# Performance work log

Hardware: AMD Instinct MI355X
Metric: run time of the kernel (lower is better)

Reference implementation:

```python
import jax, jax.numpy as jnp
import numpy as np

H = 128  # DECODER_LAYERS[0]
LN_EPS = 1e-3  # keras LayerNormalization default epsilon


def setup_inputs() -> dict:
    key = jax.random.key(0)
    ks = jax.random.split(key, 12)
    N_POS, N_COL, D = 1024, 512, 128
    n_seq = 8
    s = 1.0 / np.sqrt(D)
    h = 1.0 / np.sqrt(H)
    return {
        "seq_feat": jax.random.normal(ks[0], (N_POS, D), jnp.float32),
        "col_feat": jax.random.normal(ks[1], (N_COL, D), jnp.float32),
        "sequence_lengths": jnp.full((n_seq,), N_POS // n_seq, dtype=jnp.int32),
        "Ws": jax.random.normal(ks[2], (D, H), jnp.float32) * s,
        "bs": jnp.zeros((H,), jnp.float32),
        "Wc": jax.random.normal(ks[3], (D, H), jnp.float32) * s,
        "bc": jnp.zeros((H,), jnp.float32),
        "Wm": jax.random.normal(ks[4], (H, H), jnp.float32) * h,
        "bm": jnp.zeros((H,), jnp.float32),
        "gamma": jnp.ones((H,), jnp.float32),
        "beta": jnp.zeros((H,), jnp.float32),
        "Wo": jax.random.normal(ks[5], (H, 1), jnp.float32) * h,
        "bo": jnp.zeros((1,), jnp.float32),
    }


def reference(seq_feat, col_feat, sequence_lengths, Ws, bs, Wc, bc, Wm, bm, gamma, beta, Wo, bo):
    N_POS = seq_feat.shape[0]
    N_COL = col_feat.shape[0]
    n_seq = sequence_lengths.shape[0]

    seq_dec = jax.nn.relu(seq_feat @ Ws + bs)   # [N_pos, H]
    col_dec = jax.nn.relu(col_feat @ Wc + bc)   # [N_col, H]

    # broadcast outer-sum: [N_pos, N_col, H]
    logits = seq_dec[:, None, :] + col_dec[None, :, :]

    # MLP([128]): single Dense (no activation) + LayerNorm
    hmid = logits @ Wm + bm
    mu = jnp.mean(hmid, axis=-1, keepdims=True)
    var = jnp.mean(jnp.square(hmid - mu), axis=-1, keepdims=True)
    hln = (hmid - mu) / jnp.sqrt(var + LN_EPS) * gamma + beta

    raw = (hln @ Wo + bo)[..., 0]               # [N_pos, N_col]
    exp_logits = jnp.exp(raw)

    # column-axis normalization (softmax over last axis)
    M_c = exp_logits / jnp.sum(exp_logits, axis=-1, keepdims=True)

    # segment-ragged normalization over positions, per sequence
    segment_ids = jnp.repeat(jnp.arange(n_seq, dtype=jnp.int32), sequence_lengths,
                             total_repeat_length=N_POS)
    seg = jax.ops.segment_sum(exp_logits, segment_ids, num_segments=n_seq)  # [n_seq, N_col]
    M_s = exp_logits / seg[segment_ids]

    return M_c + M_s - M_c * M_s
```

## Files before the change

### kernel.cpp

```cpp
#include <hip/hip_runtime.h>

#define HDIM 128
#define NPOS 1024
#define NCOL 512
#define LN_EPS 1e-3f


__device__ __forceinline__ int seg_of(int i, const int* __restrict__ lens, int n_seq) {
    int cum = 0;
    for (int s = 0; s < n_seq; ++s) {
        cum += lens[s];
        if (i < cum) return s;
    }
    return n_seq - 1;
}

extern "C" __global__ void __launch_bounds__(512)
k1_precompute(const float* __restrict__ seq_feat, const float* __restrict__ col_feat,
              const float* __restrict__ Ws, const float* __restrict__ bsv,
              const float* __restrict__ Wc, const float* __restrict__ bcv,
              const float* __restrict__ Wm, const float* __restrict__ bmv,
              const float* __restrict__ gam, const float* __restrict__ Wo,
              const int* __restrict__ lens, int n_seq,
              float* __restrict__ AcT, float* __restrict__ BcT,
              float* __restrict__ p_arr, float* __restrict__ v_arr,
              float* __restrict__ q_arr, float* __restrict__ w_arr,
              float* __restrict__ sums, int* __restrict__ segid)
{
    __shared__ float xs[4][HDIM];
    __shared__ float ds_[4][HDIM];
    __shared__ float partm[8], partp[8], partv[8], mus[4];

    const int t    = threadIdx.x;
    const int b    = blockIdx.x;
    const int h    = t & 127;
    const int r    = t >> 7;
    const int wv   = t >> 6;
    const int lane = t & 63;

    {
        const int nsums = NPOS + n_seq * NCOL;
        int idx = b * 512 + t;
        if (idx < nsums) sums[idx] = 0.f;
        int idx2 = idx - nsums;
        if (idx2 >= 0 && idx2 < NPOS) segid[idx2] = seg_of(idx2, lens, n_seq);
    }

    const bool  is_seq = (b < NPOS / 4);
    const int   i0 = (is_seq ? b : (b - NPOS / 4)) * 4;
    const float* X  = is_seq ? seq_feat : col_feat;
    const float* W1 = is_seq ? Ws : Wc;
    const float* b1 = is_seq ? bsv : bcv;

    if (t < 128) {
        int rr = t >> 5, k4 = (t & 31) * 4;
        *(float4*)&xs[rr][k4] = *(const float4*)&X[(i0 + rr) * HDIM + k4];
    }
    __syncthreads();

    float d;
    {
        float a0 = 0.f, a1 = 0.f, a2 = 0.f, a3 = 0.f;
        #pragma unroll 8
        for (int k = 0; k < HDIM; k += 4) {
            float4 x = *(const float4*)&xs[r][k];
            float w0 = W1[(k + 0) * HDIM + h];
            float w1 = W1[(k + 1) * HDIM + h];
            float w2 = W1[(k + 2) * HDIM + h];
            float w3 = W1[(k + 3) * HDIM + h];
            a0 += x.x * w0; a1 += x.y * w1; a2 += x.z * w2; a3 += x.w * w3;
        }
        d = fmaxf(b1[h] + ((a0 + a1) + (a2 + a3)), 0.f);
    }
    ds_[r][h] = d;
    __syncthreads();

    float aa;
    {
        float a0 = 0.f, a1 = 0.f, a2 = 0.f, a3 = 0.f;
        #pragma unroll 8
        for (int k = 0; k < HDIM; k += 4) {
            float4 x = *(const float4*)&ds_[r][k];
            float w0 = Wm[(k + 0) * HDIM + h];
            float w1 = Wm[(k + 1) * HDIM + h];
            float w2 = Wm[(k + 2) * HDIM + h];
            float w3 = Wm[(k + 3) * HDIM + h];
            a0 += x.x * w0; a1 += x.y * w1; a2 += x.z * w2; a3 += x.w * w3;
        }
        aa = (is_seq ? 0.f : bmv[h]) + ((a0 + a1) + (a2 + a3));
    }

    {
        float s = aa;
        #pragma unroll
        for (int off = 32; off; off >>= 1) s += __shfl_xor(s, off, 64);
        if (lane == 0) partm[wv] = s;
    }
    __syncthreads();
    if (t < 4) mus[t] = (partm[2 * t] + partm[2 * t + 1]) * (1.f / HDIM);
    __syncthreads();

    const float a  = aa - mus[r];
    const float gw = gam[h] * Wo[h];

    {
        float sp = a * gw, sv = a * a;
        #pragma unroll
        for (int off = 32; off; off >>= 1) {
            sp += __shfl_xor(sp, off, 64);
            sv += __shfl_xor(sv, off, 64);
        }
        if (lane == 0) { partp[wv] = sp; partv[wv] = sv; }
    }
    xs[r][h] = a;
    __syncthreads();
    if (t < 4) {
        (is_seq ? p_arr : q_arr)[i0 + t] = partp[2 * t] + partp[2 * t + 1];
        (is_seq ? v_arr : w_arr)[i0 + t] = (partv[2 * t] + partv[2 * t + 1]) * (1.f / HDIM);
    }
    if (t < 128) {
        float4 st = make_float4(xs[0][t], xs[1][t], xs[2][t], xs[3][t]);
        if (is_seq) *(float4*)&AcT[t * NPOS + i0] = st;
        else        *(float4*)&BcT[t * NCOL + i0] = st;
    }
}

#define AS_STR 36
#define BS_STR 68

union K2Smem {
    struct { float As[128 * AS_STR]; float Bs[128 * BS_STR]; } s;
    struct { float comb[8 * 256]; float redr[512]; float redc[1024]; } r;
};

extern "C" __global__ void __launch_bounds__(512)
k2_gemm(const float* __restrict__ AcT, const float* __restrict__ BcT,
        const float* __restrict__ p_arr, const float* __restrict__ v_arr,
        const float* __restrict__ q_arr, const float* __restrict__ w_arr,
        const int* __restrict__ segid, int n_seq,
        float* __restrict__ E, float* __restrict__ rowsum, float* __restrict__ segsum)
{
    __shared__ K2Smem sm;

    const int t  = threadIdx.x;
    const int tt = t & 255;
    const int tc = tt & 15;
    const int tr = tt >> 4;
    const int kbase = (t >> 8) * 64;
    const int i0 = blockIdx.x * 32;
    const int j0 = blockIdx.y * 64;

    #pragma unroll
    for (int u = 0; u < 2; ++u) {
        int fid = t + 512 * u;
        int k = fid >> 3, m4 = fid & 7;
        *(float4*)&sm.s.As[k * AS_STR + 4 * m4] = *(const float4*)&AcT[k * NPOS + i0 + 4 * m4];
    }
    #pragma unroll
    for (int u = 0; u < 4; ++u) {
        int fid = t + 512 * u;
        int k = fid >> 4, n4 = fid & 15;
        *(float4*)&sm.s.Bs[k * BS_STR + 4 * n4] = *(const float4*)&BcT[k * NCOL + j0 + 4 * n4];
    }
    __syncthreads();

    float acc[8] = {0.f, 0.f, 0.f, 0.f, 0.f, 0.f, 0.f, 0.f};
    #pragma unroll 4
    for (int k = kbase; k < kbase + 64; ++k) {
        float2 a2 = *(const float2*)&sm.s.As[k * AS_STR + 2 * tr];
        float4 b4 = *(const float4*)&sm.s.Bs[k * BS_STR + 4 * tc];
        acc[0] += a2.x * b4.x; acc[1] += a2.x * b4.y; acc[2] += a2.x * b4.z; acc[3] += a2.x * b4.w;
        acc[4] += a2.y * b4.x; acc[5] += a2.y * b4.y; acc[6] += a2.y * b4.z; acc[7] += a2.y * b4.w;
    }

    const int seg_lo = segid[i0];
    const int seg_hi = segid[i0 + 31];
    __syncthreads();

    if (t >= 256) {
        #pragma unroll
        for (int j = 0; j < 8; ++j) sm.r.comb[j * 256 + tt] = acc[j];
    }
    __syncthreads();

    float e[2][4];
    if (t < 256) {
        #pragma unroll
        for (int j = 0; j < 8; ++j) acc[j] += sm.r.comb[j * 256 + tt];

        const int jj = j0 + 4 * tc;
        float4 q4 = *(const float4*)&q_arr[jj];
        float4 w4 = *(const float4*)&w_arr[jj];
        float rs[2];
        #pragma unroll
        for (int mm = 0; mm < 2; ++mm) {
            const int i = i0 + 2 * tr + mm;
            const float pi = p_arr[i];
            const float vi = v_arr[i];
            e[mm][0] = __expf((pi + q4.x) * rsqrtf(vi + w4.x + acc[4*mm+0] * (2.f/HDIM) + LN_EPS));
            e[mm][1] = __expf((pi + q4.y) * rsqrtf(vi + w4.y + acc[4*mm+1] * (2.f/HDIM) + LN_EPS));
            e[mm][2] = __expf((pi + q4.z) * rsqrtf(vi + w4.z + acc[4*mm+2] * (2.f/HDIM) + LN_EPS));
            e[mm][3] = __expf((pi + q4.w) * rsqrtf(vi + w4.w + acc[4*mm+3] * (2.f/HDIM) + LN_EPS));
            rs[mm] = e[mm][0] + e[mm][1] + e[mm][2] + e[mm][3];
            *(float4*)&E[i * NCOL + jj] = make_float4(e[mm][0], e[mm][1], e[mm][2], e[mm][3]);
        }
        sm.r.redr[(2 * tr + 0) * 16 + tc] = rs[0];
        sm.r.redr[(2 * tr + 1) * 16 + tc] = rs[1];
        #pragma unroll
        for (int u = 0; u < 4; ++u)
            sm.r.redc[(4 * tc + u) * 16 + tr] = e[0][u] + e[1][u];
    }
    __syncthreads();

    if (t < 32) {
        float s = 0.f;
        #pragma unroll
        for (int m = 0; m < 16; ++m) s += sm.r.redr[t * 16 + m];
        atomicAdd(&rowsum[i0 + t], s);
    } else if (t >= 32 && t < 96 && seg_lo == seg_hi) {
        int c = t - 32;
        float s = 0.f;
        #pragma unroll
        for (int m = 0; m < 16; ++m) s += sm.r.redc[c * 16 + m];
        atomicAdd(&segsum[seg_lo * NCOL + j0 + c], s);
    }
    if (seg_lo != seg_hi && t < 256) {
        #pragma unroll
        for (int mm = 0; mm < 2; ++mm) {
            const int i = i0 + 2 * tr + mm;
            const int sg = segid[i];
            #pragma unroll
            for (int u = 0; u < 4; ++u)
                atomicAdd(&segsum[sg * NCOL + j0 + 4 * tc + u], e[mm][u]);
        }
    }
}

extern "C" __global__ void __launch_bounds__(256)
k3_final(const float* __restrict__ E, const float* __restrict__ rowsum,
         const float* __restrict__ segsum, const int* __restrict__ segid,
         float* __restrict__ out)
{
    const int gid = blockIdx.x * 256 + threadIdx.x;
    const int i = gid >> 7;
    const int j = (gid & 127) * 4;

    float4 e4 = *(const float4*)&E[i * NCOL + j];
    const float invr = 1.f / rowsum[i];
    const int sg = segid[i];
    float4 s4 = *(const float4*)&segsum[sg * NCOL + j];

    float4 o;
    { float mc = e4.x * invr, ms = e4.x / s4.x; o.x = mc + ms - mc * ms; }
    { float mc = e4.y * invr, ms = e4.y / s4.y; o.y = mc + ms - mc * ms; }
    { float mc = e4.z * invr, ms = e4.z / s4.z; o.z = mc + ms - mc * ms; }
    { float mc = e4.w * invr, ms = e4.w / s4.w; o.w = mc + ms - mc * ms; }
    *(float4*)&out[i * NCOL + j] = o;
}

extern "C" void kernel_launch(void* const* d_in, const int* in_sizes, int n_in,
                              void* d_out, int out_size, void* d_ws, size_t ws_size,
                              hipStream_t stream) {
    const float* seq_feat = (const float*)d_in[0];
    const float* col_feat = (const float*)d_in[1];
    const int*   lens     = (const int*)d_in[2];
    const float* Ws   = (const float*)d_in[3];
    const float* bs   = (const float*)d_in[4];
    const float* Wc   = (const float*)d_in[5];
    const float* bc   = (const float*)d_in[6];
    const float* Wm   = (const float*)d_in[7];
    const float* bm   = (const float*)d_in[8];
    const float* gam  = (const float*)d_in[9];
    const float* Wo   = (const float*)d_in[11];
    float* out = (float*)d_out;
    const int n_seq = in_sizes[2];

    float* ws     = (float*)d_ws;
    float* AcT    = ws;
    float* BcT    = AcT + HDIM * NPOS;
    float* p      = BcT + HDIM * NCOL;
    float* v      = p + NPOS;
    float* q      = v + NPOS;
    float* w      = q + NCOL;
    float* sums   = w + NCOL;
    float* rowsum = sums;
    float* segsum = sums + NPOS;
    float* E      = segsum + n_seq * NCOL;
    int*   segid  = (int*)(E + NPOS * NCOL);

    hipLaunchKernelGGL(k1_precompute, dim3(NPOS / 4 + NCOL / 4), dim3(512), 0, stream,
                       seq_feat, col_feat, Ws, bs, Wc, bc, Wm, bm, gam, Wo,
                       lens, n_seq, AcT, BcT, p, v, q, w, sums, segid);
    hipLaunchKernelGGL(k2_gemm, dim3(NPOS / 32, NCOL / 64), dim3(512), 0, stream,
                       AcT, BcT, p, v, q, w, segid, n_seq, E, rowsum, segsum);
    hipLaunchKernelGGL(k3_final, dim3((NPOS * NCOL / 4) / 256), dim3(256), 0, stream,
                       E, rowsum, segsum, segid, out);
}
```

Measured before the change: 98.59 us.

## Fuse three kernels into one persistent kernel with atomic grid barriers

Merges the precompute, GEMM/exp and final normalization kernels into a single 256-block kernel that separates phases with a spin-wait grid barrier on a global atomic counter, reset by a memset before launch. Phase 1 loops two passes over the row units so 256 blocks cover all 384. The aim is to remove the launch gaps between kernels. In exchange it adds a memset launch and barrier spin costs, and it depends on all 256 blocks being resident at once, with no cooperative-launch guarantee.

```diff
diff --git a/kernel.cpp b/kernel.cpp
--- a/kernel.cpp
+++ b/kernel.cpp
@@ -4,258 +4,269 @@
 #define NPOS 1024
 #define NCOL 512
 #define LN_EPS 1e-3f
-
-
-__device__ __forceinline__ int seg_of(int i, const int* __restrict__ lens, int n_seq) {
-    int cum = 0;
-    for (int s = 0; s < n_seq; ++s) {
-        cum += lens[s];
-        if (i < cum) return s;
-    }
-    return n_seq - 1;
-}
-
-extern "C" __global__ void __launch_bounds__(512)
-k1_precompute(const float* __restrict__ seq_feat, const float* __restrict__ col_feat,
-              const float* __restrict__ Ws, const float* __restrict__ bsv,
-              const float* __restrict__ Wc, const float* __restrict__ bcv,
-              const float* __restrict__ Wm, const float* __restrict__ bmv,
-              const float* __restrict__ gam, const float* __restrict__ Wo,
-              const int* __restrict__ lens, int n_seq,
-              float* __restrict__ AcT, float* __restrict__ BcT,
-              float* __restrict__ p_arr, float* __restrict__ v_arr,
-              float* __restrict__ q_arr, float* __restrict__ w_arr,
-              float* __restrict__ sums, int* __restrict__ segid)
-{
-    __shared__ float xs[4][HDIM];
-    __shared__ float ds_[4][HDIM];
-    __shared__ float partm[8], partp[8], partv[8], mus[4];
-
-    const int t    = threadIdx.x;
-    const int b    = blockIdx.x;
-    const int h    = t & 127;
-    const int r    = t >> 7;
-    const int wv   = t >> 6;
-    const int lane = t & 63;
-
-    {
-        const int nsums = NPOS + n_seq * NCOL;
-        int idx = b * 512 + t;
-        if (idx < nsums) sums[idx] = 0.f;
-        int idx2 = idx - nsums;
-        if (idx2 >= 0 && idx2 < NPOS) segid[idx2] = seg_of(idx2, lens, n_seq);
-    }
-
-    const bool  is_seq = (b < NPOS / 4);
-    const int   i0 = (is_seq ? b : (b - NPOS / 4)) * 4;
-    const float* X  = is_seq ? seq_feat : col_feat;
-    const float* W1 = is_seq ? Ws : Wc;
-    const float* b1 = is_seq ? bsv : bcv;
-
-    if (t < 128) {
-        int rr = t >> 5, k4 = (t & 31) * 4;
-        *(float4*)&xs[rr][k4] = *(const float4*)&X[(i0 + rr) * HDIM + k4];
-    }
-    __syncthreads();
-
-    float d;
-    {
-        float a0 = 0.f, a1 = 0.f, a2 = 0.f, a3 = 0.f;
-        #pragma unroll 8
-        for (int k = 0; k < HDIM; k += 4) {
-            float4 x = *(const float4*)&xs[r][k];
-            float w0 = W1[(k + 0) * HDIM + h];
-            float w1 = W1[(k + 1) * HDIM + h];
-            float w2 = W1[(k + 2) * HDIM + h];
-            float w3 = W1[(k + 3) * HDIM + h];
-            a0 += x.x * w0; a1 += x.y * w1; a2 += x.z * w2; a3 += x.w * w3;
-        }
-        d = fmaxf(b1[h] + ((a0 + a1) + (a2 + a3)), 0.f);
-    }
-    ds_[r][h] = d;
-    __syncthreads();
-
-    float aa;
-    {
-        float a0 = 0.f, a1 = 0.f, a2 = 0.f, a3 = 0.f;
-        #pragma unroll 8
-        for (int k = 0; k < HDIM; k += 4) {
-            float4 x = *(const float4*)&ds_[r][k];
-            float w0 = Wm[(k + 0) * HDIM + h];
-            float w1 = Wm[(k + 1) * HDIM + h];
-            float w2 = Wm[(k + 2) * HDIM + h];
-            float w3 = Wm[(k + 3) * HDIM + h];
-            a0 += x.x * w0; a1 += x.y * w1; a2 += x.z * w2; a3 += x.w * w3;
-        }
-        aa = (is_seq ? 0.f : bmv[h]) + ((a0 + a1) + (a2 + a3));
-    }
-
-    {
-        float s = aa;
-        #pragma unroll
-        for (int off = 32; off; off >>= 1) s += __shfl_xor(s, off, 64);
-        if (lane == 0) partm[wv] = s;
-    }
-    __syncthreads();
-    if (t < 4) mus[t] = (partm[2 * t] + partm[2 * t + 1]) * (1.f / HDIM);
-    __syncthreads();
-
-    const float a  = aa - mus[r];
-    const float gw = gam[h] * Wo[h];
-
-    {
-        float sp = a * gw, sv = a * a;
-        #pragma unroll
-        for (int off = 32; off; off >>= 1) {
-            sp += __shfl_xor(sp, off, 64);
-            sv += __shfl_xor(sv, off, 64);
-        }
-        if (lane == 0) { partp[wv] = sp; partv[wv] = sv; }
-    }
-    xs[r][h] = a;
-    __syncthreads();
-    if (t < 4) {
-        (is_seq ? p_arr : q_arr)[i0 + t] = partp[2 * t] + partp[2 * t + 1];
-        (is_seq ? v_arr : w_arr)[i0 + t] = (partv[2 * t] + partv[2 * t + 1]) * (1.f / HDIM);
-    }
-    if (t < 128) {
-        float4 st = make_float4(xs[0][t], xs[1][t], xs[2][t], xs[3][t]);
-        if (is_seq) *(float4*)&AcT[t * NPOS + i0] = st;
-        else        *(float4*)&BcT[t * NCOL + i0] = st;
-    }
-}
+#define NBLK 256
+
 
 #define AS_STR 36
 #define BS_STR 68
 
-union K2Smem {
+union FusedSmem {
+    struct {
+        float xs[4][HDIM];
+        float ds[4][HDIM];
+        float partm[8], partp[8], partv[8], mus[4];
+    } p1;
     struct { float As[128 * AS_STR]; float Bs[128 * BS_STR]; } s;
     struct { float comb[8 * 256]; float redr[512]; float redc[1024]; } r;
 };
 
-extern "C" __global__ void __launch_bounds__(512)
-k2_gemm(const float* __restrict__ AcT, const float* __restrict__ BcT,
-        const float* __restrict__ p_arr, const float* __restrict__ v_arr,
-        const float* __restrict__ q_arr, const float* __restrict__ w_arr,
-        const int* __restrict__ segid, int n_seq,
-        float* __restrict__ E, float* __restrict__ rowsum, float* __restrict__ segsum)
-{
-    __shared__ K2Smem sm;
-
-    const int t  = threadIdx.x;
-    const int tt = t & 255;
-    const int tc = tt & 15;
-    const int tr = tt >> 4;
-    const int kbase = (t >> 8) * 64;
-    const int i0 = blockIdx.x * 32;
-    const int j0 = blockIdx.y * 64;
-
-    #pragma unroll
-    for (int u = 0; u < 2; ++u) {
-        int fid = t + 512 * u;
-        int k = fid >> 3, m4 = fid & 7;
-        *(float4*)&sm.s.As[k * AS_STR + 4 * m4] = *(const float4*)&AcT[k * NPOS + i0 + 4 * m4];
-    }
-    #pragma unroll
-    for (int u = 0; u < 4; ++u) {
-        int fid = t + 512 * u;
-        int k = fid >> 4, n4 = fid & 15;
-        *(float4*)&sm.s.Bs[k * BS_STR + 4 * n4] = *(const float4*)&BcT[k * NCOL + j0 + 4 * n4];
+__device__ __forceinline__ int seg_of(int i, const int* __restrict__ lens, int n_seq) {
+    int cum = 0;
+    for (int s = 0; s < n_seq; ++s) { cum += lens[s]; if (i < cum) return s; }
+    return n_seq - 1;
+}
+
+__device__ __forceinline__ void grid_sync(unsigned int* bar, unsigned int need) {
+    __syncthreads();
+    if (threadIdx.x == 0) {
+        __hip_atomic_fetch_add(bar, 1u, __ATOMIC_RELEASE, __HIP_MEMORY_SCOPE_AGENT);
+        while (__hip_atomic_load(bar, __ATOMIC_ACQUIRE, __HIP_MEMORY_SCOPE_AGENT) < need) {}
     }
     __syncthreads();
-
-    float acc[8] = {0.f, 0.f, 0.f, 0.f, 0.f, 0.f, 0.f, 0.f};
-    #pragma unroll 4
-    for (int k = kbase; k < kbase + 64; ++k) {
-        float2 a2 = *(const float2*)&sm.s.As[k * AS_STR + 2 * tr];
-        float4 b4 = *(const float4*)&sm.s.Bs[k * BS_STR + 4 * tc];
-        acc[0] += a2.x * b4.x; acc[1] += a2.x * b4.y; acc[2] += a2.x * b4.z; acc[3] += a2.x * b4.w;
-        acc[4] += a2.y * b4.x; acc[5] += a2.y * b4.y; acc[6] += a2.y * b4.z; acc[7] += a2.y * b4.w;
+}
+
+extern "C" __global__ void __launch_bounds__(512, 2)
+fused_all(const float* __restrict__ seq_feat, const float* __restrict__ col_feat,
+          const float* __restrict__ Ws, const float* __restrict__ bsv,
+          const float* __restrict__ Wc, const float* __restrict__ bcv,
+          const float* __restrict__ Wm, const float* __restrict__ bmv,
+          const float* __restrict__ gam, const float* __restrict__ Wo,
+          const int* __restrict__ lens, int n_seq,
+          float* __restrict__ AcT, float* __restrict__ BcT,
+          float* __restrict__ p_arr, float* __restrict__ v_arr,
+          float* __restrict__ q_arr, float* __restrict__ w_arr,
+          float* __restrict__ sums, int* __restrict__ segid,
+          float* __restrict__ E, float* __restrict__ out,
+          unsigned int* __restrict__ bar)
+{
+    __shared__ FusedSmem sm;
+    const int t = threadIdx.x;
+    const int b = blockIdx.x;
+
+    {
+        const int h    = t & 127;
+        const int r    = t >> 7;
+        const int wv   = t >> 6;
+        const int lane = t & 63;
+
+        {
+            const int nsums = NPOS + n_seq * NCOL;
+            int idx = b * 512 + t;
+            if (idx < nsums) sums[idx] = 0.f;
+            int idx2 = idx - nsums;
+            if (idx2 >= 0 && idx2 < NPOS) segid[idx2] = seg_of(idx2, lens, n_seq);
+        }
+
+        for (int pass = 0; pass < 2; ++pass) {
+            const int unit = b + NBLK * pass;
+            if (unit < (NPOS + NCOL) / 4) {
+                const bool  is_seq = (unit < NPOS / 4);
+                const int   i0 = (is_seq ? unit : unit - NPOS / 4) * 4;
+                const float* X  = is_seq ? seq_feat : col_feat;
+                const float* W1 = is_seq ? Ws : Wc;
+                const float* b1 = is_seq ? bsv : bcv;
+
+                if (t < 128) {
+                    int rr = t >> 5, k4 = (t & 31) * 4;
+                    *(float4*)&sm.p1.xs[rr][k4] = *(const float4*)&X[(i0 + rr) * HDIM + k4];
+                }
+                __syncthreads();
+
+                float d;
+                {
+                    float a0 = 0.f, a1 = 0.f, a2 = 0.f, a3 = 0.f;
+                    #pragma unroll 8
+                    for (int k = 0; k < HDIM; k += 4) {
+                        float4 x = *(const float4*)&sm.p1.xs[r][k];
+                        float w0 = W1[(k + 0) * HDIM + h];
+                        float w1 = W1[(k + 1) * HDIM + h];
+                        float w2 = W1[(k + 2) * HDIM + h];
+                        float w3 = W1[(k + 3) * HDIM + h];
+                        a0 += x.x * w0; a1 += x.y * w1; a2 += x.z * w2; a3 += x.w * w3;
+                    }
+                    d = fmaxf(b1[h] + ((a0 + a1) + (a2 + a3)), 0.f);
+                }
+                sm.p1.ds[r][h] = d;
+                __syncthreads();
+
+                float aa;
+                {
+                    float a0 = 0.f, a1 = 0.f, a2 = 0.f, a3 = 0.f;
+                    #pragma unroll 8
+                    for (int k = 0; k < HDIM; k += 4) {
+                        float4 x = *(const float4*)&sm.p1.ds[r][k];
+                        float w0 = Wm[(k + 0) * HDIM + h];
+                        float w1 = Wm[(k + 1) * HDIM + h];
+                        float w2 = Wm[(k + 2) * HDIM + h];
+                        float w3 = Wm[(k + 3) * HDIM + h];
+                        a0 += x.x * w0; a1 += x.y * w1; a2 += x.z * w2; a3 += x.w * w3;
+                    }
+                    aa = (is_seq ? 0.f : bmv[h]) + ((a0 + a1) + (a2 + a3));
+                }
+
+                {
+                    float s = aa;
+                    #pragma unroll
+                    for (int off = 32; off; off >>= 1) s += __shfl_xor(s, off, 64);
+                    if (lane == 0) sm.p1.partm[wv] = s;
+                }
+                __syncthreads();
+                if (t < 4) sm.p1.mus[t] = (sm.p1.partm[2 * t] + sm.p1.partm[2 * t + 1]) * (1.f / HDIM);
+                __syncthreads();
+
+                const float a  = aa - sm.p1.mus[r];
+                const float gw = gam[h] * Wo[h];
+
+                {
+                    float sp = a * gw, sv = a * a;
+                    #pragma unroll
+                    for (int off = 32; off; off >>= 1) {
+                        sp += __shfl_xor(sp, off, 64);
+                        sv += __shfl_xor(sv, off, 64);
+                    }
+                    if (lane == 0) { sm.p1.partp[wv] = sp; sm.p1.partv[wv] = sv; }
+                }
+                sm.p1.xs[r][h] = a;
+                __syncthreads();
+                if (t < 4) {
+                    (is_seq ? p_arr : q_arr)[i0 + t] = sm.p1.partp[2 * t] + sm.p1.partp[2 * t + 1];
+                    (is_seq ? v_arr : w_arr)[i0 + t] = (sm.p1.partv[2 * t] + sm.p1.partv[2 * t + 1]) * (1.f / HDIM);
+                }
+                if (t < 128) {
+                    float4 st = make_float4(sm.p1.xs[0][t], sm.p1.xs[1][t], sm.p1.xs[2][t], sm.p1.xs[3][t]);
+                    if (is_seq) *(float4*)&AcT[t * NPOS + i0] = st;
+                    else        *(float4*)&BcT[t * NCOL + i0] = st;
+                }
+            }
+            __syncthreads();
+        }
     }
-
-    const int seg_lo = segid[i0];
-    const int seg_hi = segid[i0 + 31];
-    __syncthreads();
-
-    if (t >= 256) {
+    grid_sync(bar, 1u * NBLK);
+
+    float* rowsum = sums;
+    float* segsum = sums + NPOS;
+    {
+        const int tt = t & 255;
+        const int tc = tt & 15;
+        const int tr = tt >> 4;
+        const int kbase = (t >> 8) * 64;
+        const int i0 = (b >> 3) * 32;
+        const int j0 = (b & 7) * 64;
+
         #pragma unroll
-        for (int j = 0; j < 8; ++j) sm.r.comb[j * 256 + tt] = acc[j];
+        for (int u = 0; u < 2; ++u) {
+            int fid = t + 512 * u;
+            int k = fid >> 3, m4 = fid & 7;
+            *(float4*)&sm.s.As[k * AS_STR + 4 * m4] = *(const float4*)&AcT[k * NPOS + i0 + 4 * m4];
+        }
+        #pragma unroll
+        for (int u = 0; u < 4; ++u) {
+            int fid = t + 512 * u;
+            int k = fid >> 4, n4 = fid & 15;
+            *(float4*)&sm.s.Bs[k * BS_STR + 4 * n4] = *(const float4*)&BcT[k * NCOL + j0 + 4 * n4];
+        }
+        __syncthreads();
+
+        float acc[8] = {0.f, 0.f, 0.f, 0.f, 0.f, 0.f, 0.f, 0.f};
+        #pragma unroll 4
+        for (int k = kbase; k < kbase + 64; ++k) {
+            float2 a2 = *(const float2*)&sm.s.As[k * AS_STR + 2 * tr];
+            float4 b4 = *(const float4*)&sm.s.Bs[k * BS_STR + 4 * tc];
+            acc[0] += a2.x * b4.x; acc[1] += a2.x * b4.y; acc[2] += a2.x * b4.z; acc[3] += a2.x * b4.w;
+            acc[4] += a2.y * b4.x; acc[5] += a2.y * b4.y; acc[6] += a2.y * b4.z; acc[7] += a2.y * b4.w;
+        }
+
+        const int seg_lo = segid[i0];
+        const int seg_hi = segid[i0 + 31];
+        __syncthreads();
+
+        if (t >= 256) {
+            #pragma unroll
+            for (int j = 0; j < 8; ++j) sm.r.comb[j * 256 + tt] = acc[j];
+        }
+        __syncthreads();
+
+        float e[2][4];
+        if (t < 256) {
+            #pragma unroll
+            for (int j = 0; j < 8; ++j) acc[j] += sm.r.comb[j * 256 + tt];
+
+            const int jj = j0 + 4 * tc;
+            float4 q4 = *(const float4*)&q_arr[jj];
+            float4 w4 = *(const float4*)&w_arr[jj];
+            float rs[2];
+            #pragma unroll
+            for (int mm = 0; mm < 2; ++mm) {
+                const int i = i0 + 2 * tr + mm;
+                const float pi = p_arr[i];
+                const float vi = v_arr[i];
+                e[mm][0] = __expf((pi + q4.x) * rsqrtf(vi + w4.x + acc[4*mm+0] * (2.f/HDIM) + LN_EPS));
+                e[mm][1] = __expf((pi + q4.y) * rsqrtf(vi + w4.y + acc[4*mm+1] * (2.f/HDIM) + LN_EPS));
+                e[mm][2] = __expf((pi + q4.z) * rsqrtf(vi + w4.z + acc[4*mm+2] * (2.f/HDIM) + LN_EPS));
+                e[mm][3] = __expf((pi + q4.w) * rsqrtf(vi + w4.w + acc[4*mm+3] * (2.f/HDIM) + LN_EPS));
+                rs[mm] = e[mm][0] + e[mm][1] + e[mm][2] + e[mm][3];
+                *(float4*)&E[i * NCOL + jj] = make_float4(e[mm][0], e[mm][1], e[mm][2], e[mm][3]);
+            }
+            sm.r.redr[(2 * tr + 0) * 16 + tc] = rs[0];
+            sm.r.redr[(2 * tr + 1) * 16 + tc] = rs[1];
+            #pragma unroll
+            for (int u = 0; u < 4; ++u)
+                sm.r.redc[(4 * tc + u) * 16 + tr] = e[0][u] + e[1][u];
+        }
+        __syncthreads();
+
+        if (t < 32) {
+            float s = 0.f;
+            #pragma unroll
+            for (int m = 0; m < 16; ++m) s += sm.r.redr[t * 16 + m];
+            atomicAdd(&rowsum[i0 + t], s);
+        } else if (t >= 32 && t < 96 && seg_lo == seg_hi) {
+            int c = t - 32;
+            float s = 0.f;
+            #pragma unroll
+            for (int m = 0; m < 16; ++m) s += sm.r.redc[c * 16 + m];
+            atomicAdd(&segsum[seg_lo * NCOL + j0 + c], s);
+        }
+        if (seg_lo != seg_hi && t < 256) {
+            #pragma unroll
+            for (int mm = 0; mm < 2; ++mm) {
+                const int i = i0 + 2 * tr + mm;
+                const int sg = segid[i];
+                #pragma unroll
+                for (int u = 0; u < 4; ++u)
+                    atomicAdd(&segsum[sg * NCOL + j0 + 4 * tc + u], e[mm][u]);
+            }
+        }
     }
-    __syncthreads();
-
-    float e[2][4];
-    if (t < 256) {
-        #pragma unroll
-        for (int j = 0; j < 8; ++j) acc[j] += sm.r.comb[j * 256 + tt];
-
-        const int jj = j0 + 4 * tc;
-        float4 q4 = *(const float4*)&q_arr[jj];
-        float4 w4 = *(const float4*)&w_arr[jj];
-        float rs[2];
-        #pragma unroll
-        for (int mm = 0; mm < 2; ++mm) {
-            const int i = i0 + 2 * tr + mm;
-            const float pi = p_arr[i];
-            const float vi = v_arr[i];
-            e[mm][0] = __expf((pi + q4.x) * rsqrtf(vi + w4.x + acc[4*mm+0] * (2.f/HDIM) + LN_EPS));
-            e[mm][1] = __expf((pi + q4.y) * rsqrtf(vi + w4.y + acc[4*mm+1] * (2.f/HDIM) + LN_EPS));
-            e[mm][2] = __expf((pi + q4.z) * rsqrtf(vi + w4.z + acc[4*mm+2] * (2.f/HDIM) + LN_EPS));
-            e[mm][3] = __expf((pi + q4.w) * rsqrtf(vi + w4.w + acc[4*mm+3] * (2.f/HDIM) + LN_EPS));
-            rs[mm] = e[mm][0] + e[mm][1] + e[mm][2] + e[mm][3];
-            *(float4*)&E[i * NCOL + jj] = make_float4(e[mm][0], e[mm][1], e[mm][2], e[mm][3]);
-        }
-        sm.r.redr[(2 * tr + 0) * 16 + tc] = rs[0];
-        sm.r.redr[(2 * tr + 1) * 16 + tc] = rs[1];
-        #pragma unroll
-        for (int u = 0; u < 4; ++u)
-            sm.r.redc[(4 * tc + u) * 16 + tr] = e[0][u] + e[1][u];
+    grid_sync(bar, 2u * NBLK);
+
+    {
+        const int gid = b * 512 + t;
+        const int i = gid >> 7;
+        const int j = (gid & 127) * 4;
+
+        float4 e4 = *(const float4*)&E[i * NCOL + j];
+        const float invr = 1.f / rowsum[i];
+        const int sg = segid[i];
+        float4 s4 = *(const float4*)&segsum[sg * NCOL + j];
+
+        float4 o;
+        { float mc = e4.x * invr, ms = e4.x / s4.x; o.x = mc + ms - mc * ms; }
+        { float mc = e4.y * invr, ms = e4.y / s4.y; o.y = mc + ms - mc * ms; }
+        { float mc = e4.z * invr, ms = e4.z / s4.z; o.z = mc + ms - mc * ms; }
+        { float mc = e4.w * invr, ms = e4.w / s4.w; o.w = mc + ms - mc * ms; }
+        *(float4*)&out[i * NCOL + j] = o;
     }
-    __syncthreads();
-
-    if (t < 32) {
-        float s = 0.f;
-        #pragma unroll
-        for (int m = 0; m < 16; ++m) s += sm.r.redr[t * 16 + m];
-        atomicAdd(&rowsum[i0 + t], s);
-    } else if (t >= 32 && t < 96 && seg_lo == seg_hi) {
-        int c = t - 32;
-        float s = 0.f;
-        #pragma unroll
-        for (int m = 0; m < 16; ++m) s += sm.r.redc[c * 16 + m];
-        atomicAdd(&segsum[seg_lo * NCOL + j0 + c], s);
-    }
-    if (seg_lo != seg_hi && t < 256) {
-        #pragma unroll
-        for (int mm = 0; mm < 2; ++mm) {
-            const int i = i0 + 2 * tr + mm;
-            const int sg = segid[i];
-            #pragma unroll
-            for (int u = 0; u < 4; ++u)
-                atomicAdd(&segsum[sg * NCOL + j0 + 4 * tc + u], e[mm][u]);
-        }
-    }
-}
-
-extern "C" __global__ void __launch_bounds__(256)
-k3_final(const float* __restrict__ E, const float* __restrict__ rowsum,
-         const float* __restrict__ segsum, const int* __restrict__ segid,
-         float* __restrict__ out)
-{
-    const int gid = blockIdx.x * 256 + threadIdx.x;
-    const int i = gid >> 7;
-    const int j = (gid & 127) * 4;
-
-    float4 e4 = *(const float4*)&E[i * NCOL + j];
-    const float invr = 1.f / rowsum[i];
-    const int sg = segid[i];
-    float4 s4 = *(const float4*)&segsum[sg * NCOL + j];
-
-    float4 o;
-    { float mc = e4.x * invr, ms = e4.x / s4.x; o.x = mc + ms - mc * ms; }
-    { float mc = e4.y * invr, ms = e4.y / s4.y; o.y = mc + ms - mc * ms; }
-    { float mc = e4.z * invr, ms = e4.z / s4.z; o.z = mc + ms - mc * ms; }
-    { float mc = e4.w * invr, ms = e4.w / s4.w; o.w = mc + ms - mc * ms; }
-    *(float4*)&out[i * NCOL + j] = o;
 }
 
 extern "C" void kernel_launch(void* const* d_in, const int* in_sizes, int n_in,
@@ -283,16 +294,12 @@
     float* q      = v + NPOS;
     float* w      = q + NCOL;
     float* sums   = w + NCOL;
-    float* rowsum = sums;
-    float* segsum = sums + NPOS;
-    float* E      = segsum + n_seq * NCOL;
+    float* E      = sums + NPOS + n_seq * NCOL;
     int*   segid  = (int*)(E + NPOS * NCOL);
-
-    hipLaunchKernelGGL(k1_precompute, dim3(NPOS / 4 + NCOL / 4), dim3(512), 0, stream,
+    unsigned int* bar = (unsigned int*)(segid + NPOS);
+
+    hipMemsetAsync(bar, 0, sizeof(unsigned int), stream);
+    hipLaunchKernelGGL(fused_all, dim3(NBLK), dim3(512), 0, stream,
                        seq_feat, col_feat, Ws, bs, Wc, bc, Wm, bm, gam, Wo,
-                       lens, n_seq, AcT, BcT, p, v, q, w, sums, segid);
-    hipLaunchKernelGGL(k2_gemm, dim3(NPOS / 32, NCOL / 64), dim3(512), 0, stream,
-                       AcT, BcT, p, v, q, w, segid, n_seq, E, rowsum, segsum);
-    hipLaunchKernelGGL(k3_final, dim3((NPOS * NCOL / 4) / 256), dim3(256), 0, stream,
-                       E, rowsum, segsum, segid, out);
+                       lens, n_seq, AcT, BcT, p, v, q, w, sums, segid, E, out, bar);
 }
```

Result: slower. 135.7 us (+37.6%).
